# Kernel tuning notes

Measured on AMD Instinct MI355X. Metric: run time of the kernel, lower is better.

The kernel has to match this reference:

```python
import jax, jax.numpy as jnp
import numpy as np

N = 50000      # nodes
E = 800000     # edges (before self-loops)
DIN, DH, DOUT = 128, 64, 64


def setup_inputs() -> dict:
    key = jax.random.key(0)
    ks = jax.random.split(key, 8)
    x = jax.random.normal(ks[0], (N, DIN), dtype=jnp.float32)
    edge_index = jax.random.randint(ks[1], (2, E), 0, N, dtype=jnp.int64)
    W1 = jax.random.normal(ks[2], (DIN, DH), dtype=jnp.float32) / np.sqrt(DIN)
    b1 = jnp.zeros((DH,), dtype=jnp.float32)
    W2 = jax.random.normal(ks[3], (DH, DOUT), dtype=jnp.float32) / np.sqrt(DH)
    b2 = jnp.zeros((DOUT,), dtype=jnp.float32)
    Wfc = jax.random.normal(ks[4], (DOUT, DOUT), dtype=jnp.float32) / np.sqrt(DOUT)
    bfc = jnp.zeros((DOUT,), dtype=jnp.float32)
    return {"x": x, "edge_index": edge_index, "W1": W1, "b1": b1,
            "W2": W2, "b2": b2, "Wfc": Wfc, "bfc": bfc}


def _gcn_conv(x, W, b, src, dst, n):
    # PyG GCNConv: h = x @ W; symmetric normalization with self-loops;
    # aggregate messages norm * h[src] into dst; add bias.
    h = x @ W                                              # [n, d_out]
    ones = jnp.ones(src.shape[0], dtype=h.dtype)
    deg = jax.ops.segment_sum(ones, dst, num_segments=n)   # in-degree incl. self-loops
    dinv = jnp.where(deg > 0, jax.lax.rsqrt(deg), 0.0)
    norm = dinv[src] * dinv[dst]                           # [E+n]
    msg = h[src] * norm[:, None]                           # gather + scale
    out = jax.ops.segment_sum(msg, dst, num_segments=n)    # scatter-add
    return out + b


def reference(x, edge_index, W1, b1, W2, b2, Wfc, bfc):
    n = x.shape[0]
    loops = jnp.arange(n, dtype=edge_index.dtype)
    src = jnp.concatenate([edge_index[0], loops])
    dst = jnp.concatenate([edge_index[1], loops])
    h = jax.nn.relu(_gcn_conv(x, W1, b1, src, dst, n))
    h = _gcn_conv(h, W2, b2, src, dst, n)
    return h @ Wfc + bfc
```

## Files before the change

### kernel.cpp

```cpp
#include <hip/hip_runtime.h>

#define THREADS 256
#define DIN 128
#define SB 256
#define BSTRIDE 64
#define NCHUNK 256
#define BCAP 16384

typedef _Float16 half_t;
typedef __attribute__((ext_vector_type(4))) _Float16 half4;

__device__ __forceinline__ void fma4(float4& a, const float4& w, float s) {
  a.x = fmaf(w.x, s, a.x);
  a.y = fmaf(w.y, s, a.y);
  a.z = fmaf(w.z, s, a.z);
  a.w = fmaf(w.w, s, a.w);
}

__device__ __forceinline__ void fma4h(float4& a, const half4& h, float s) {
  a.x = fmaf((float)h[0], s, a.x);
  a.y = fmaf((float)h[1], s, a.y);
  a.z = fmaf((float)h[2], s, a.z);
  a.w = fmaf((float)h[3], s, a.w);
}

__global__ void k_zero_i(int* __restrict__ p, int n) {
  int i = blockIdx.x * blockDim.x + threadIdx.x;
  if (i < n) p[i] = 0;
}

__global__ __launch_bounds__(THREADS) void k_binfill_gemm1(
    const int* __restrict__ src, const int* __restrict__ dst,
    unsigned int* __restrict__ ebuf, int* __restrict__ binCur,
    int E, int CH, int nbin,
    const float* __restrict__ in, const float* __restrict__ W,
    half_t* __restrict__ out, int n, int ngemm) {
  __shared__ int lhist[256];
  __shared__ int lbase[256];
  __shared__ float Ws[DIN][64];
  const int t = threadIdx.x;
  if ((int)blockIdx.x < NCHUNK) {
    const int chunk = blockIdx.x;
    lhist[t] = 0;
    __syncthreads();
    const int lo = chunk * CH;
    const int hi = min(lo + CH, E);
    const int m = hi - lo;
    const int nv = (m > 0) ? (m >> 2) : 0;
    for (int g = t; g < nv; g += THREADS) {
      int4 d4 = *reinterpret_cast<const int4*>(dst + lo + (g << 2));
      atomicAdd(&lhist[d4.x >> 8], 1);
      atomicAdd(&lhist[d4.y >> 8], 1);
      atomicAdd(&lhist[d4.z >> 8], 1);
      atomicAdd(&lhist[d4.w >> 8], 1);
    }
    for (int e = lo + (nv << 2) + t; e < hi; e += THREADS)
      atomicAdd(&lhist[dst[e] >> 8], 1);
    __syncthreads();
    if (t < nbin) {
      int c = lhist[t];
      lbase[t] = (c > 0) ? atomicAdd(&binCur[t], c) : 0;
    }
    __syncthreads();
    for (int g = t; g < nv; g += THREADS) {
      const int base = lo + (g << 2);
      int4 d4 = *reinterpret_cast<const int4*>(dst + base);
      int4 s4 = *reinterpret_cast<const int4*>(src + base);
      int bin, pos;
      bin = d4.x >> 8; pos = atomicAdd(&lbase[bin], 1);
      if (pos < BCAP) ebuf[(size_t)bin * BCAP + pos] =
          ((unsigned int)(d4.x & 255) << 16) | (unsigned int)s4.x;
      bin = d4.y >> 8; pos = atomicAdd(&lbase[bin], 1);
      if (pos < BCAP) ebuf[(size_t)bin * BCAP + pos] =
          ((unsigned int)(d4.y & 255) << 16) | (unsigned int)s4.y;
      bin = d4.z >> 8; pos = atomicAdd(&lbase[bin], 1);
      if (pos < BCAP) ebuf[(size_t)bin * BCAP + pos] =
          ((unsigned int)(d4.z & 255) << 16) | (unsigned int)s4.z;
      bin = d4.w >> 8; pos = atomicAdd(&lbase[bin], 1);
      if (pos < BCAP) ebuf[(size_t)bin * BCAP + pos] =
          ((unsigned int)(d4.w & 255) << 16) | (unsigned int)s4.w;
    }
    for (int e = lo + (nv << 2) + t; e < hi; e += THREADS) {
      int d = dst[e];
      int s = src[e];
      int bin = d >> 8;
      int pos = atomicAdd(&lbase[bin], 1);
      if (pos < BCAP)
        ebuf[(size_t)bin * BCAP + pos] =
            ((unsigned int)(d & 255) << 16) | (unsigned int)s;
    }
  } else {
    for (int i = t; i < DIN * 64; i += THREADS) Ws[i >> 6][i & 63] = W[i];
    __syncthreads();
    const int c = (t & 15) << 2;
    const int rs = t >> 4;
    const int gb = (int)blockIdx.x - NCHUNK;
    for (int row0 = gb * 64; row0 < n; row0 += ngemm * 64) {
      const int r0 = row0 + rs * 4;
      const float* xp[4];
#pragma unroll
      for (int j = 0; j < 4; ++j) {
        int row = r0 + j;
        if (row >= n) row = n - 1;
        xp[j] = in + (size_t)row * DIN;
      }
      float4 acc[4];
#pragma unroll
      for (int j = 0; j < 4; ++j) acc[j] = make_float4(0.f, 0.f, 0.f, 0.f);
#pragma unroll 4
      for (int k = 0; k < DIN; k += 4) {
        float4 w0 = *reinterpret_cast<const float4*>(&Ws[k + 0][c]);
        float4 w1 = *reinterpret_cast<const float4*>(&Ws[k + 1][c]);
        float4 w2 = *reinterpret_cast<const float4*>(&Ws[k + 2][c]);
        float4 w3 = *reinterpret_cast<const float4*>(&Ws[k + 3][c]);
#pragma unroll
        for (int j = 0; j < 4; ++j) {
          float4 xv = *reinterpret_cast<const float4*>(xp[j] + k);
          fma4(acc[j], w0, xv.x);
          fma4(acc[j], w1, xv.y);
          fma4(acc[j], w2, xv.z);
          fma4(acc[j], w3, xv.w);
        }
      }
#pragma unroll
      for (int j = 0; j < 4; ++j) {
        int row = r0 + j;
        if (row < n) {
          half4 hv;
          hv[0] = (half_t)acc[j].x; hv[1] = (half_t)acc[j].y;
          hv[2] = (half_t)acc[j].z; hv[3] = (half_t)acc[j].w;
          *reinterpret_cast<half4*>(&out[(size_t)row * 64 + c]) = hv;
        }
      }
    }
  }
}

__global__ __launch_bounds__(THREADS) void k_bucket_build(
    const unsigned int* __restrict__ ebuf, const int* __restrict__ binCur,
    unsigned short* __restrict__ colb, int* __restrict__ cnt,
    float* __restrict__ dinv, int n) {
  __shared__ int lcnt[256];
  __shared__ __align__(16) unsigned short lcol[256 * BSTRIDE];
  const int t = threadIdx.x;
  const int p = blockIdx.x;
  lcnt[t] = 0;
  __syncthreads();
  const int bc = min(binCur[p], BCAP);
  const size_t seg = (size_t)p * BCAP;
  const int nv = bc >> 2;
  for (int g = t; g < nv; g += THREADS) {
    uint4 pk4 = *reinterpret_cast<const uint4*>(&ebuf[seg + ((size_t)g << 2)]);
    int dl, pos;
    dl = (int)(pk4.x >> 16); pos = atomicAdd(&lcnt[dl], 1);
    if (pos < BSTRIDE) lcol[(dl << 6) + pos] = (unsigned short)(pk4.x & 0xffffu);
    dl = (int)(pk4.y >> 16); pos = atomicAdd(&lcnt[dl], 1);
    if (pos < BSTRIDE) lcol[(dl << 6) + pos] = (unsigned short)(pk4.y & 0xffffu);
    dl = (int)(pk4.z >> 16); pos = atomicAdd(&lcnt[dl], 1);
    if (pos < BSTRIDE) lcol[(dl << 6) + pos] = (unsigned short)(pk4.z & 0xffffu);
    dl = (int)(pk4.w >> 16); pos = atomicAdd(&lcnt[dl], 1);
    if (pos < BSTRIDE) lcol[(dl << 6) + pos] = (unsigned short)(pk4.w & 0xffffu);
  }
  for (int i = (nv << 2) + t; i < bc; i += THREADS) {
    unsigned int pk = ebuf[seg + i];
    int dl = (int)(pk >> 16);
    int pos = atomicAdd(&lcnt[dl], 1);
    if (pos < BSTRIDE) lcol[(dl << 6) + pos] = (unsigned short)(pk & 0xffffu);
  }
  __syncthreads();
  const int node0 = p << 8;
  const int nn = min(256, n - node0);
  if (t < nn) {
    cnt[node0 + t] = lcnt[t];
    dinv[node0 + t] = rsqrtf((float)(lcnt[t] + 1));
  }
  const uint4* ls = reinterpret_cast<const uint4*>(lcol);
  uint4* gd = reinterpret_cast<uint4*>(colb + ((size_t)node0 << 6));
  const int nvv = nn << 3;
  for (int i = t; i < nvv; i += THREADS) gd[i] = ls[i];
}

template<bool RELU_Z, bool OUT_BIAS, bool OUT_HALF>
__global__ __launch_bounds__(THREADS) void k_gather_mm(
    const int* __restrict__ cnt, const float* __restrict__ dinv,
    const unsigned short* __restrict__ colb, const half_t* __restrict__ h,
    const float* __restrict__ bias_agg, const float* __restrict__ Wmm,
    const float* __restrict__ bias_out, void* __restrict__ outp, int n) {
  __shared__ __align__(16) float Ws[64][64];
  __shared__ __align__(16) float rowbuf[4][4][64];
  for (int i = threadIdx.x; i < 64 * 64; i += THREADS) Ws[i >> 6][i & 63] = Wmm[i];
  __syncthreads();

  const int wid = threadIdx.x >> 6;
  const int s = (threadIdx.x >> 4) & 3;
  const int cc = (threadIdx.x & 15) << 2;
  const int g = blockIdx.x * 16 + (threadIdx.x >> 4);

  if (g < n) {
    const int cg = cnt[g];
    const int beg = g * BSTRIDE;
    const int end = beg + min(cg, BSTRIDE);

    float4 a0 = make_float4(0.f, 0.f, 0.f, 0.f);
    float4 a1 = a0, a2 = a0, a3 = a0;
    int j = beg;
    for (; j + 4 <= end; j += 4) {
      ushort4 c4 = *reinterpret_cast<const ushort4*>(&colb[j]);
      float w0 = dinv[c4.x], w1 = dinv[c4.y], w2 = dinv[c4.z], w3 = dinv[c4.w];
      half4 h0 = *reinterpret_cast<const half4*>(&h[(size_t)c4.x * 64 + cc]);
      half4 h1 = *reinterpret_cast<const half4*>(&h[(size_t)c4.y * 64 + cc]);
      half4 h2 = *reinterpret_cast<const half4*>(&h[(size_t)c4.z * 64 + cc]);
      half4 h3 = *reinterpret_cast<const half4*>(&h[(size_t)c4.w * 64 + cc]);
      fma4h(a0, h0, w0);
      fma4h(a1, h1, w1);
      fma4h(a2, h2, w2);
      fma4h(a3, h3, w3);
    }
    for (; j < end; ++j) {
      int sc = colb[j];
      float w0 = dinv[sc];
      half4 h0 = *reinterpret_cast<const half4*>(&h[(size_t)sc * 64 + cc]);
      fma4h(a0, h0, w0);
    }
    a0.x += a1.x + a2.x + a3.x;
    a0.y += a1.y + a2.y + a3.y;
    a0.z += a1.z + a2.z + a3.z;
    a0.w += a1.w + a2.w + a3.w;

    const float di = dinv[g];
    const float di2 = di * di;
    half4 hs = *reinterpret_cast<const half4*>(&h[(size_t)g * 64 + cc]);
    float4 bv = *reinterpret_cast<const float4*>(&bias_agg[cc]);
    float4 z;
    z.x = fmaf(a0.x, di, fmaf((float)hs[0], di2, bv.x));
    z.y = fmaf(a0.y, di, fmaf((float)hs[1], di2, bv.y));
    z.z = fmaf(a0.z, di, fmaf((float)hs[2], di2, bv.z));
    z.w = fmaf(a0.w, di, fmaf((float)hs[3], di2, bv.w));
    if (RELU_Z) {
      z.x = fmaxf(z.x, 0.f); z.y = fmaxf(z.y, 0.f);
      z.z = fmaxf(z.z, 0.f); z.w = fmaxf(z.w, 0.f);
    }
    *reinterpret_cast<float4*>(&rowbuf[wid][s][cc]) = z;

    float4 acc = OUT_BIAS ? *reinterpret_cast<const float4*>(&bias_out[cc])
                          : make_float4(0.f, 0.f, 0.f, 0.f);
#pragma unroll
    for (int k = 0; k < 64; k += 4) {
      float4 zk = *reinterpret_cast<const float4*>(&rowbuf[wid][s][k]);
      fma4(acc, *reinterpret_cast<const float4*>(&Ws[k + 0][cc]), zk.x);
      fma4(acc, *reinterpret_cast<const float4*>(&Ws[k + 1][cc]), zk.y);
      fma4(acc, *reinterpret_cast<const float4*>(&Ws[k + 2][cc]), zk.z);
      fma4(acc, *reinterpret_cast<const float4*>(&Ws[k + 3][cc]), zk.w);
    }
    if (OUT_HALF) {
      half4 ov;
      ov[0] = (half_t)acc.x; ov[1] = (half_t)acc.y;
      ov[2] = (half_t)acc.z; ov[3] = (half_t)acc.w;
      *reinterpret_cast<half4*>(&((half_t*)outp)[(size_t)g * 64 + cc]) = ov;
    } else {
      *reinterpret_cast<float4*>(&((float*)outp)[(size_t)g * 64 + cc]) = acc;
    }
  }
}

__global__ void k_count(const int* __restrict__ dst, int* __restrict__ deg, int E) {
  int e = blockIdx.x * blockDim.x + threadIdx.x;
  if (e < E) atomicAdd(&deg[dst[e]], 1);
}

__global__ __launch_bounds__(SB) void k_scan1(const int* __restrict__ deg,
                                              int* __restrict__ row_ptr,
                                              int* __restrict__ blockSum,
                                              float* __restrict__ dinv, int n) {
  __shared__ int tmp[SB];
  const int t = threadIdx.x;
  const int i = blockIdx.x * SB + t;
  int v = (i < n) ? deg[i] : 0;
  tmp[t] = v;
  __syncthreads();
#pragma unroll
  for (int off = 1; off < SB; off <<= 1) {
    int u = (t >= off) ? tmp[t - off] : 0;
    __syncthreads();
    tmp[t] += u;
    __syncthreads();
  }
  if (i < n) {
    row_ptr[i] = tmp[t] - v;
    dinv[i] = rsqrtf((float)(v + 1));
  }
  if (t == SB - 1) blockSum[blockIdx.x] = tmp[SB - 1];
}

__global__ __launch_bounds__(SB) void k_scan2(int* __restrict__ blockSum, int nb) {
  __shared__ int tmp[SB];
  const int t = threadIdx.x;
  const int chunk = (nb + SB - 1) / SB;
  const int lo = t * chunk;
  const int hi = min(lo + chunk, nb);
  int s = 0;
  for (int i = lo; i < hi; ++i) s += blockSum[i];
  tmp[t] = s;
  __syncthreads();
#pragma unroll
  for (int off = 1; off < SB; off <<= 1) {
    int u = (t >= off) ? tmp[t - off] : 0;
    __syncthreads();
    tmp[t] += u;
    __syncthreads();
  }
  int run = tmp[t] - s;
  for (int i = lo; i < hi; ++i) {
    int v = blockSum[i];
    blockSum[i] = run;
    run += v;
  }
}

__global__ __launch_bounds__(SB) void k_scan3(int* __restrict__ row_ptr,
                                              const int* __restrict__ blockSum,
                                              int* __restrict__ cursor, int n, int E) {
  const int i = blockIdx.x * SB + threadIdx.x;
  if (i < n) {
    int r = row_ptr[i] + blockSum[blockIdx.x];
    row_ptr[i] = r;
    cursor[i] = r;
  }
  if (i == 0) row_ptr[n] = E;
}

__global__ void k_fill_csr(const int* __restrict__ src, const int* __restrict__ dst,
                           int* __restrict__ cursor, int* __restrict__ col, int E) {
  int e = blockIdx.x * blockDim.x + threadIdx.x;
  if (e >= E) return;
  int pos = atomicAdd(&cursor[dst[e]], 1);
  col[pos] = src[e];
}

template<int K, bool RELU_IN, bool ADD_BIAS>
__global__ __launch_bounds__(THREADS) void k_gemm(
    const float* in, const float* __restrict__ W,
    const float* __restrict__ bias, float* out, int n) {
  __shared__ float Ws[K][64];
  for (int i = threadIdx.x; i < K * 64; i += THREADS) Ws[i >> 6][i & 63] = W[i];
  __syncthreads();
  const int c = (threadIdx.x & 15) << 2;
  const int rs = threadIdx.x >> 4;
  for (int row0 = blockIdx.x * 64; row0 < n; row0 += gridDim.x * 64) {
    const int r0 = row0 + rs * 4;
    const float* xp[4];
#pragma unroll
    for (int j = 0; j < 4; ++j) {
      int row = r0 + j;
      if (row >= n) row = n - 1;
      xp[j] = in + (size_t)row * K;
    }
    float4 acc[4];
#pragma unroll
    for (int j = 0; j < 4; ++j) acc[j] = make_float4(0.f, 0.f, 0.f, 0.f);
#pragma unroll 4
    for (int k = 0; k < K; k += 4) {
      float4 w0 = *reinterpret_cast<const float4*>(&Ws[k + 0][c]);
      float4 w1 = *reinterpret_cast<const float4*>(&Ws[k + 1][c]);
      float4 w2 = *reinterpret_cast<const float4*>(&Ws[k + 2][c]);
      float4 w3 = *reinterpret_cast<const float4*>(&Ws[k + 3][c]);
#pragma unroll
      for (int j = 0; j < 4; ++j) {
        float4 xv = *reinterpret_cast<const float4*>(xp[j] + k);
        if (RELU_IN) {
          xv.x = fmaxf(xv.x, 0.f); xv.y = fmaxf(xv.y, 0.f);
          xv.z = fmaxf(xv.z, 0.f); xv.w = fmaxf(xv.w, 0.f);
        }
        fma4(acc[j], w0, xv.x);
        fma4(acc[j], w1, xv.y);
        fma4(acc[j], w2, xv.z);
        fma4(acc[j], w3, xv.w);
      }
    }
#pragma unroll
    for (int j = 0; j < 4; ++j) {
      int row = r0 + j;
      if (row < n) {
        float4 o = acc[j];
        if (ADD_BIAS) {
          const float4 bv = *reinterpret_cast<const float4*>(&bias[c]);
          o.x += bv.x; o.y += bv.y; o.z += bv.z; o.w += bv.w;
        }
        *reinterpret_cast<float4*>(&out[(size_t)row * 64 + c]) = o;
      }
    }
  }
}

__global__ __launch_bounds__(THREADS) void k_gather_csr(
    const int* __restrict__ row_ptr, const int* __restrict__ col,
    const float* __restrict__ h, const float* __restrict__ dinv,
    const float* __restrict__ bias, float* __restrict__ out, int n) {
  int g = blockIdx.x * (THREADS / 16) + (threadIdx.x >> 4);
  if (g >= n) return;
  const int cc = (threadIdx.x & 15) << 2;
  int beg = row_ptr[g];
  int end = row_ptr[g + 1];
  float4 acc0 = make_float4(0.f, 0.f, 0.f, 0.f);
  float4 acc1 = make_float4(0.f, 0.f, 0.f, 0.f);
  int j = beg;
  for (; j + 2 <= end; j += 2) {
    int s0 = col[j], s1 = col[j + 1];
    float w0 = dinv[s0], w1 = dinv[s1];
    float4 h0 = *reinterpret_cast<const float4*>(&h[(size_t)s0 * 64 + cc]);
    float4 h1 = *reinterpret_cast<const float4*>(&h[(size_t)s1 * 64 + cc]);
    fma4(acc0, h0, w0);
    fma4(acc1, h1, w1);
  }
  if (j < end) {
    int s0 = col[j];
    float w0 = dinv[s0];
    float4 h0 = *reinterpret_cast<const float4*>(&h[(size_t)s0 * 64 + cc]);
    fma4(acc0, h0, w0);
  }
  acc0.x += acc1.x; acc0.y += acc1.y; acc0.z += acc1.z; acc0.w += acc1.w;
  const float di = dinv[g];
  const float di2 = di * di;
  float4 hv = *reinterpret_cast<const float4*>(&h[(size_t)g * 64 + cc]);
  float4 bv = *reinterpret_cast<const float4*>(&bias[cc]);
  float4 o;
  o.x = fmaf(acc0.x, di, fmaf(hv.x, di2, bv.x));
  o.y = fmaf(acc0.y, di, fmaf(hv.y, di2, bv.y));
  o.z = fmaf(acc0.z, di, fmaf(hv.z, di2, bv.z));
  o.w = fmaf(acc0.w, di, fmaf(hv.w, di2, bv.w));
  *reinterpret_cast<float4*>(&out[(size_t)g * 64 + cc]) = o;
}

extern "C" void kernel_launch(void* const* d_in, const int* in_sizes, int n_in,
                              void* d_out, int out_size, void* d_ws, size_t ws_size,
                              hipStream_t stream) {
  const float* x = (const float*)d_in[0];
  const int* ei = (const int*)d_in[1];
  const float* W1 = (const float*)d_in[2];
  const float* b1 = (const float*)d_in[3];
  const float* W2 = (const float*)d_in[4];
  const float* b2 = (const float*)d_in[5];
  const float* Wfc = (const float*)d_in[6];
  const float* bfc = (const float*)d_in[7];
  float* out = (float*)d_out;

  const int n = in_sizes[0] / DIN;
  const int E = in_sizes[1] / 2;
  const int* srcp = ei;
  const int* dstp = ei + E;

  const int gn = (n + THREADS - 1) / THREADS;
  const int ge = (E + THREADS - 1) / THREADS;
  const int ggemm = (n + 63) / 64;

  const int nbin = (n + 255) >> 8;
  const int CH = (((E + NCHUNK - 1) / NCHUNK) + 3) & ~3;

  const size_t need_binned = (size_t)n * 392 +
                             (size_t)nbin * (BCAP + 1) * 4 + 1024;

  if (n <= 65535 && nbin <= 256 && ws_size >= need_binned) {
    char* w = (char*)d_ws;
    half_t* h1 = (half_t*)w;            w += (size_t)n * 64 * 2;
    half_t* h2 = (half_t*)w;            w += (size_t)n * 64 * 2;
    unsigned short* colb = (unsigned short*)w;  w += (size_t)n * BSTRIDE * 2;
    unsigned int* ebuf = (unsigned int*)w;      w += (size_t)nbin * BCAP * 4;
    int* binCur = (int*)w;              w += (size_t)(nbin + 16) * 4;
    int* cnt = (int*)w;                 w += (size_t)n * 4;
    float* dinv = (float*)w;

    const int ggat = (n + 15) / 16;

    k_zero_i<<<1, THREADS, 0, stream>>>(binCur, nbin);
    k_binfill_gemm1<<<NCHUNK + ggemm, THREADS, 0, stream>>>(
        srcp, dstp, ebuf, binCur, E, CH, nbin, x, W1, h1, n, ggemm);
    k_bucket_build<<<nbin, THREADS, 0, stream>>>(ebuf, binCur, colb, cnt, dinv, n);
    k_gather_mm<true, false, true><<<ggat, THREADS, 0, stream>>>(
        cnt, dinv, colb, h1, b1, W2, nullptr, h2, n);
    k_gather_mm<false, true, false><<<ggat, THREADS, 0, stream>>>(
        cnt, dinv, colb, h2, b2, Wfc, bfc, out, n);
  } else {
    const int nb = (n + SB - 1) / SB;
    char* w = (char*)d_ws;
    float* dinv = (float*)w;   w += (size_t)n * 4;
    float* bufA = (float*)w;   w += (size_t)n * 64 * 4;
    int* deg = (int*)w;        w += (size_t)n * 4;
    int* row_ptr = (int*)w;    w += (size_t)(n + 4) * 4;
    int* cursor = (int*)w;     w += (size_t)n * 4;
    int* blockSum = (int*)w;   w += (size_t)(nb + 4) * 4;
    int* col = (int*)w;

    k_zero_i<<<gn, THREADS, 0, stream>>>(deg, n);
    k_count<<<ge, THREADS, 0, stream>>>(dstp, deg, E);
    k_scan1<<<nb, SB, 0, stream>>>(deg, row_ptr, blockSum, dinv, n);
    k_scan2<<<1, SB, 0, stream>>>(blockSum, nb);
    k_scan3<<<nb, SB, 0, stream>>>(row_ptr, blockSum, cursor, n, E);
    k_fill_csr<<<ge, THREADS, 0, stream>>>(srcp, dstp, cursor, col, E);

    const int ggat16 = (n + 15) / 16;
    k_gemm<DIN, false, false><<<ggemm, THREADS, 0, stream>>>(x, W1, nullptr, bufA, n);
    k_gather_csr<<<ggat16, THREADS, 0, stream>>>(row_ptr, col, bufA, dinv, b1, out, n);
    k_gemm<64, true, false><<<ggemm, THREADS, 0, stream>>>(out, W2, nullptr, bufA, n);
    k_gather_csr<<<ggat16, THREADS, 0, stream>>>(row_ptr, col, bufA, dinv, b2, out, n);
    k_gemm<64, false, true><<<ggemm, THREADS, 0, stream>>>(out, Wfc, bfc, out, n);
  }
  (void)n_in; (void)out_size;
}
```

Before: 98.68 us.

## Prescale second-layer features by dinv and store gather weights in half

The first gather kernel now multiplies its output rows by the source node's dinv before storing, so the second gather can do plain adds and skip the per-edge dinv lookups. The gather loop also prefetches the next group of column indices before doing the loads for the current group. The shared-memory weight matrix is converted to fp16, which halves LDS use and load traffic but adds rounding error to the dense 64x64 matmul.

Result: faster. 94.54 us, median of 2 (-4.2%).

```diff
diff --git a/kernel.cpp b/kernel.cpp
--- a/kernel.cpp
+++ b/kernel.cpp
@@ -22,6 +22,20 @@
   a.y = fmaf((float)h[1], s, a.y);
   a.z = fmaf((float)h[2], s, a.z);
   a.w = fmaf((float)h[3], s, a.w);
+}
+
+__device__ __forceinline__ void add4h(float4& a, const half4& h) {
+  a.x += (float)h[0];
+  a.y += (float)h[1];
+  a.z += (float)h[2];
+  a.w += (float)h[3];
+}
+
+__device__ __forceinline__ void fma4hw(float4& a, const half4& w, float s) {
+  a.x = fmaf((float)w[0], s, a.x);
+  a.y = fmaf((float)w[1], s, a.y);
+  a.z = fmaf((float)w[2], s, a.z);
+  a.w = fmaf((float)w[3], s, a.w);
 }
 
 __global__ void k_zero_i(int* __restrict__ p, int n) {
@@ -180,15 +194,21 @@
   for (int i = t; i < nvv; i += THREADS) gd[i] = ls[i];
 }
 
-template<bool RELU_Z, bool OUT_BIAS, bool OUT_HALF>
+template<bool RELU_Z, bool OUT_BIAS, bool OUT_HALF, bool IN_PRESCALED, bool PRESCALE_OUT>
 __global__ __launch_bounds__(THREADS) void k_gather_mm(
     const int* __restrict__ cnt, const float* __restrict__ dinv,
     const unsigned short* __restrict__ colb, const half_t* __restrict__ h,
     const float* __restrict__ bias_agg, const float* __restrict__ Wmm,
     const float* __restrict__ bias_out, void* __restrict__ outp, int n) {
-  __shared__ __align__(16) float Ws[64][64];
+  __shared__ __align__(16) half_t Wsh[64 * 64];
   __shared__ __align__(16) float rowbuf[4][4][64];
-  for (int i = threadIdx.x; i < 64 * 64; i += THREADS) Ws[i >> 6][i & 63] = Wmm[i];
+  for (int i = threadIdx.x; i < 1024; i += THREADS) {
+    float4 wv = reinterpret_cast<const float4*>(Wmm)[i];
+    half4 hv;
+    hv[0] = (half_t)wv.x; hv[1] = (half_t)wv.y;
+    hv[2] = (half_t)wv.z; hv[3] = (half_t)wv.w;
+    reinterpret_cast<half4*>(Wsh)[i] = hv;
+  }
   __syncthreads();
 
   const int wid = threadIdx.x >> 6;
@@ -204,23 +224,36 @@
     float4 a0 = make_float4(0.f, 0.f, 0.f, 0.f);
     float4 a1 = a0, a2 = a0, a3 = a0;
     int j = beg;
-    for (; j + 4 <= end; j += 4) {
+    if (j + 4 <= end) {
       ushort4 c4 = *reinterpret_cast<const ushort4*>(&colb[j]);
-      float w0 = dinv[c4.x], w1 = dinv[c4.y], w2 = dinv[c4.z], w3 = dinv[c4.w];
-      half4 h0 = *reinterpret_cast<const half4*>(&h[(size_t)c4.x * 64 + cc]);
-      half4 h1 = *reinterpret_cast<const half4*>(&h[(size_t)c4.y * 64 + cc]);
-      half4 h2 = *reinterpret_cast<const half4*>(&h[(size_t)c4.z * 64 + cc]);
-      half4 h3 = *reinterpret_cast<const half4*>(&h[(size_t)c4.w * 64 + cc]);
-      fma4h(a0, h0, w0);
-      fma4h(a1, h1, w1);
-      fma4h(a2, h2, w2);
-      fma4h(a3, h3, w3);
+      while (j + 4 <= end) {
+        ushort4 nx = c4;
+        if (j + 8 <= end) nx = *reinterpret_cast<const ushort4*>(&colb[j + 4]);
+        half4 h0 = *reinterpret_cast<const half4*>(&h[(size_t)c4.x * 64 + cc]);
+        half4 h1 = *reinterpret_cast<const half4*>(&h[(size_t)c4.y * 64 + cc]);
+        half4 h2 = *reinterpret_cast<const half4*>(&h[(size_t)c4.z * 64 + cc]);
+        half4 h3 = *reinterpret_cast<const half4*>(&h[(size_t)c4.w * 64 + cc]);
+        if (IN_PRESCALED) {
+          add4h(a0, h0);
+          add4h(a1, h1);
+          add4h(a2, h2);
+          add4h(a3, h3);
+        } else {
+          float w0 = dinv[c4.x], w1 = dinv[c4.y], w2 = dinv[c4.z], w3 = dinv[c4.w];
+          fma4h(a0, h0, w0);
+          fma4h(a1, h1, w1);
+          fma4h(a2, h2, w2);
+          fma4h(a3, h3, w3);
+        }
+        c4 = nx;
+        j += 4;
+      }
     }
     for (; j < end; ++j) {
       int sc = colb[j];
-      float w0 = dinv[sc];
       half4 h0 = *reinterpret_cast<const half4*>(&h[(size_t)sc * 64 + cc]);
-      fma4h(a0, h0, w0);
+      if (IN_PRESCALED) add4h(a0, h0);
+      else fma4h(a0, h0, dinv[sc]);
     }
     a0.x += a1.x + a2.x + a3.x;
     a0.y += a1.y + a2.y + a3.y;
@@ -228,14 +261,21 @@
     a0.w += a1.w + a2.w + a3.w;
 
     const float di = dinv[g];
-    const float di2 = di * di;
     half4 hs = *reinterpret_cast<const half4*>(&h[(size_t)g * 64 + cc]);
     float4 bv = *reinterpret_cast<const float4*>(&bias_agg[cc]);
     float4 z;
-    z.x = fmaf(a0.x, di, fmaf((float)hs[0], di2, bv.x));
-    z.y = fmaf(a0.y, di, fmaf((float)hs[1], di2, bv.y));
-    z.z = fmaf(a0.z, di, fmaf((float)hs[2], di2, bv.z));
-    z.w = fmaf(a0.w, di, fmaf((float)hs[3], di2, bv.w));
+    if (IN_PRESCALED) {
+      z.x = fmaf(a0.x + (float)hs[0], di, bv.x);
+      z.y = fmaf(a0.y + (float)hs[1], di, bv.y);
+      z.z = fmaf(a0.z + (float)hs[2], di, bv.z);
+      z.w = fmaf(a0.w + (float)hs[3], di, bv.w);
+    } else {
+      const float di2 = di * di;
+      z.x = fmaf(a0.x, di, fmaf((float)hs[0], di2, bv.x));
+      z.y = fmaf(a0.y, di, fmaf((float)hs[1], di2, bv.y));
+      z.z = fmaf(a0.z, di, fmaf((float)hs[2], di2, bv.z));
+      z.w = fmaf(a0.w, di, fmaf((float)hs[3], di2, bv.w));
+    }
     if (RELU_Z) {
       z.x = fmaxf(z.x, 0.f); z.y = fmaxf(z.y, 0.f);
       z.z = fmaxf(z.z, 0.f); z.w = fmaxf(z.w, 0.f);
@@ -247,10 +287,13 @@
 #pragma unroll
     for (int k = 0; k < 64; k += 4) {
       float4 zk = *reinterpret_cast<const float4*>(&rowbuf[wid][s][k]);
-      fma4(acc, *reinterpret_cast<const float4*>(&Ws[k + 0][cc]), zk.x);
-      fma4(acc, *reinterpret_cast<const float4*>(&Ws[k + 1][cc]), zk.y);
-      fma4(acc, *reinterpret_cast<const float4*>(&Ws[k + 2][cc]), zk.z);
-      fma4(acc, *reinterpret_cast<const float4*>(&Ws[k + 3][cc]), zk.w);
+      fma4hw(acc, *reinterpret_cast<const half4*>(&Wsh[(k + 0) * 64 + cc]), zk.x);
+      fma4hw(acc, *reinterpret_cast<const half4*>(&Wsh[(k + 1) * 64 + cc]), zk.y);
+      fma4hw(acc, *reinterpret_cast<const half4*>(&Wsh[(k + 2) * 64 + cc]), zk.z);
+      fma4hw(acc, *reinterpret_cast<const half4*>(&Wsh[(k + 3) * 64 + cc]), zk.w);
+    }
+    if (PRESCALE_OUT) {
+      acc.x *= di; acc.y *= di; acc.z *= di; acc.w *= di;
     }
     if (OUT_HALF) {
       half4 ov;
@@ -475,9 +518,9 @@
     k_binfill_gemm1<<<NCHUNK + ggemm, THREADS, 0, stream>>>(
         srcp, dstp, ebuf, binCur, E, CH, nbin, x, W1, h1, n, ggemm);
     k_bucket_build<<<nbin, THREADS, 0, stream>>>(ebuf, binCur, colb, cnt, dinv, n);
-    k_gather_mm<true, false, true><<<ggat, THREADS, 0, stream>>>(
+    k_gather_mm<true, false, true, false, true><<<ggat, THREADS, 0, stream>>>(
         cnt, dinv, colb, h1, b1, W2, nullptr, h2, n);
-    k_gather_mm<false, true, false><<<ggat, THREADS, 0, stream>>>(
+    k_gather_mm<false, true, false, true, false><<<ggat, THREADS, 0, stream>>>(
         cnt, dinv, colb, h2, b2, Wfc, bfc, out, n);
   } else {
     const int nb = (n + SB - 1) / SB;
```
